# Kernel tuning notes

Hardware: AMD Instinct MI355X
Metric: run time of the kernel (lower is better)

## Reference

```python
import jax, jax.numpy as jnp
import numpy as np

NUM_EXPERTS = 64
TOP_K = 8
NUM_TOKENS = 8192
HIDDEN = 1024
INTER = 512


def setup_inputs() -> dict:
    key = jax.random.key(0)
    k1, k2, k3, k4 = jax.random.split(key, 4)
    # 0.02 scale keeps activations in a sane range (randn weights with fan-in 1024)
    return {
        "hidden_states": jax.random.normal(k1, (NUM_TOKENS, HIDDEN), jnp.float32),
        "router_weight": jax.random.normal(k2, (HIDDEN, NUM_EXPERTS), jnp.float32) * 0.02,
        "merged_gate_up_proj": jax.random.normal(k3, (NUM_EXPERTS, HIDDEN, 2 * INTER), jnp.float32) * 0.02,
        "merged_down_proj": jax.random.normal(k4, (NUM_EXPERTS, INTER, HIDDEN), jnp.float32) * 0.02,
    }


def reference(hidden_states, router_weight, merged_gate_up_proj, merged_down_proj):
    T, H = hidden_states.shape
    E = router_weight.shape[1]

    # ---- Router: softmax over experts, top-k, renormalize top-k weights ----
    logits = hidden_states @ router_weight                       # [T, E]
    probs = jax.nn.softmax(logits, axis=-1)
    routing_weights, routing_indices = jax.lax.top_k(probs, TOP_K)  # [T, k]
    routing_weights = routing_weights / routing_weights.sum(-1, keepdims=True)

    # ---- Permute (haojun_permute_topk): replicate tokens topk times, stable-sort by expert ----
    flat_indices = routing_indices.reshape(-1)                   # [T*k]
    sort_order = jnp.argsort(flat_indices)                       # stable sort
    flat_states = jnp.repeat(hidden_states, TOP_K, axis=0)       # [T*k, H]
    permuted = flat_states[sort_order]                           # tokens grouped by expert
    group_sizes = jnp.bincount(flat_indices, length=E).astype(jnp.int32)  # tokens per expert

    # ---- Grouped MLP (grouped_gemm.gmm equivalent): y_i = x_i @ W[expert(i)] ----
    merged = jax.lax.ragged_dot(permuted, merged_gate_up_proj, group_sizes)  # [T*k, 2*I]
    gate, up = jnp.split(merged, 2, axis=-1)
    h = jax.nn.silu(gate) * up                                   # SiLU-gated (hidden_act='silu')
    expert_out = jax.lax.ragged_dot(h, merged_down_proj, group_sizes)        # [T*k, H]

    # ---- Unpermute: invert the sort, weight by routing probs, sum over top-k ----
    inv = jnp.argsort(sort_order)                                # unsort_order
    unpermuted = expert_out[inv].reshape(T, TOP_K, H)
    return (unpermuted * routing_weights[..., None]).sum(axis=1)  # [T, H]
```

## Files before the change

### kernel.cpp

```cpp
#include <hip/hip_runtime.h>
#include <cstdint>
#include <cstddef>

typedef __bf16 bf16_t;
typedef __bf16 bf16x8 __attribute__((ext_vector_type(8)));
typedef __bf16 bf16x4 __attribute__((ext_vector_type(4)));
typedef float f32x4 __attribute__((ext_vector_type(4)));

#define T_TOKENS 8192
#define HID 1024
#define INTER 512
#define NEXP 64
#define TOPK 8
#define NROWS (T_TOKENS * TOPK)
#define RT_TOK 16

typedef const unsigned int __attribute__((address_space(1)))* gptr_t;
typedef unsigned int __attribute__((address_space(3)))* lptr_t;

__device__ __forceinline__ void gload_lds16(const void* g, void* l) {
  __builtin_amdgcn_global_load_lds((gptr_t)g, (lptr_t)l, 16, 0, 0);
}

__device__ __forceinline__ f32x4 mfma16(bf16x8 a, bf16x8 b, f32x4 c) {
  return __builtin_amdgcn_mfma_f32_16x16x32_bf16(a, b, c, 0, 0, 0);
}

__device__ __forceinline__ int xcd_swizzle(int bid, int nwg) {
  int q = nwg >> 3;
  int xcd = bid & 7, i = bid >> 3;
  return xcd * q + i;
}

__global__ void transpose_cvt_kernel(const float* __restrict__ W, bf16_t* __restrict__ Wt,
                                     int K, int N) {
  const int e = blockIdx.z;
  const int n0 = blockIdx.x * 64, k0 = blockIdx.y * 64;
  const int tid = threadIdx.x;
  __shared__ __align__(8) bf16_t tile[64][68];
  {
    const int r = tid >> 2, cq = tid & 3;
    const float* src = W + ((size_t)e * K + k0 + r) * N + n0 + cq * 16;
#pragma unroll
    for (int q = 0; q < 4; ++q) {
      float4 v = *(const float4*)(src + q * 4);
      bf16x4 b;
      b[0] = (bf16_t)v.x; b[1] = (bf16_t)v.y; b[2] = (bf16_t)v.z; b[3] = (bf16_t)v.w;
      *(bf16x4*)&tile[r][cq * 16 + q * 4] = b;
    }
  }
  __syncthreads();
  {
    const int nl = tid >> 2, kq = tid & 3;
    __align__(16) bf16_t tmp[16];
#pragma unroll
    for (int i = 0; i < 16; ++i) tmp[i] = tile[kq * 16 + i][nl];
    bf16_t* dst = Wt + ((size_t)e * N + n0 + nl) * K + k0 + kq * 16;
    *(bf16x8*)(dst + 0) = *(const bf16x8*)(tmp + 0);
    *(bf16x8*)(dst + 8) = *(const bf16x8*)(tmp + 8);
  }
}

__global__ void cvt_bf16_kernel(const float* __restrict__ in, bf16_t* __restrict__ out, int n4) {
  int i = blockIdx.x * blockDim.x + threadIdx.x;
  if (i < n4) {
    float4 v = ((const float4*)in)[i];
    bf16x4 o;
    o[0] = (bf16_t)v.x; o[1] = (bf16_t)v.y; o[2] = (bf16_t)v.z; o[3] = (bf16_t)v.w;
    ((bf16x4*)out)[i] = o;
  }
}

__launch_bounds__(256, 2)
__global__ void router_kernel(const float* __restrict__ hs, const float* __restrict__ rw,
                              float* __restrict__ wval, int* __restrict__ widx) {
  const int t0 = blockIdx.x * RT_TOK;
  const int tid = threadIdx.x;
  const int lane = tid & 63, w = tid >> 6;
  __shared__ float hsl[RT_TOK][HID / 4][4];
  __shared__ float part[4][RT_TOK][NEXP];

  for (int i = tid; i < RT_TOK * (HID / 4); i += 256) {
    int t = i >> 8, c = i & 255;
    *(float4*)&hsl[t][c][0] = ((const float4*)(hs + (size_t)(t0 + t) * HID))[c];
  }
  __syncthreads();

  float acc[RT_TOK];
#pragma unroll
  for (int t = 0; t < RT_TOK; ++t) acc[t] = 0.f;
  const int kb = w * 256;
  for (int kc = 0; kc < 64; ++kc) {
    const int k = kb + kc * 4;
    float r0 = rw[(size_t)(k + 0) * NEXP + lane];
    float r1 = rw[(size_t)(k + 1) * NEXP + lane];
    float r2 = rw[(size_t)(k + 2) * NEXP + lane];
    float r3 = rw[(size_t)(k + 3) * NEXP + lane];
#pragma unroll
    for (int t = 0; t < RT_TOK; ++t) {
      float4 hv = *(const float4*)&hsl[t][(kb >> 2) + kc][0];
      acc[t] = fmaf(hv.x, r0, acc[t]);
      acc[t] = fmaf(hv.y, r1, acc[t]);
      acc[t] = fmaf(hv.z, r2, acc[t]);
      acc[t] = fmaf(hv.w, r3, acc[t]);
    }
  }
#pragma unroll
  for (int t = 0; t < RT_TOK; ++t) part[w][t][lane] = acc[t];
  __syncthreads();

  for (int j = 0; j < 4; ++j) {
    const int t = w * 4 + j;
    float logit = part[0][t][lane] + part[1][t][lane] + part[2][t][lane] + part[3][t][lane];
    float m = logit;
    for (int off = 32; off; off >>= 1) m = fmaxf(m, __shfl_xor(m, off));
    float ex = expf(logit - m);
    float Z = ex;
    for (int off = 32; off; off >>= 1) Z += __shfl_xor(Z, off);
    float p = ex / Z;
    float sum8 = 0.f;
    float outv[8]; int outi[8];
#pragma unroll
    for (int s = 0; s < 8; ++s) {
      float v = p; int idx = lane;
      for (int off = 32; off; off >>= 1) {
        float vv = __shfl_xor(v, off);
        int ii = __shfl_xor(idx, off);
        if (vv > v || (vv == v && ii < idx)) { v = vv; idx = ii; }
      }
      outv[s] = v; outi[s] = idx; sum8 += v;
      if (lane == idx) p = -1.f;
    }
    if (lane == 0) {
      float inv = 1.f / sum8;
#pragma unroll
      for (int s = 0; s < 8; ++s) {
        wval[(size_t)(t0 + t) * TOPK + s] = outv[s] * inv;
        widx[(size_t)(t0 + t) * TOPK + s] = outi[s];
      }
    }
  }
}

__global__ void hist_kernel(const int* __restrict__ widx, int* __restrict__ cnt) {
  __shared__ int h[NEXP];
  if (threadIdx.x < NEXP) h[threadIdx.x] = 0;
  __syncthreads();
  for (int i = blockIdx.x * blockDim.x + threadIdx.x; i < NROWS; i += gridDim.x * blockDim.x)
    atomicAdd(&h[widx[i]], 1);
  __syncthreads();
  if (threadIdx.x < NEXP) atomicAdd(&cnt[threadIdx.x], h[threadIdx.x]);
}

__global__ void scan_kernel(const int* __restrict__ cnt, int* __restrict__ seg,
                            int* __restrict__ cnt2) {
  if (threadIdx.x == 0) {
    int a = 0;
    for (int e2 = 0; e2 < NEXP; ++e2) { seg[e2] = a; a += cnt[e2]; }
    seg[NEXP] = a;
  }
  if (threadIdx.x < NEXP) cnt2[threadIdx.x] = 0;
}

__global__ void assign_kernel(const int* __restrict__ widx, const int* __restrict__ seg,
                              int* __restrict__ cnt2, int* __restrict__ row_org) {
  for (int i = blockIdx.x * blockDim.x + threadIdx.x; i < NROWS; i += gridDim.x * blockDim.x) {
    int e = widx[i];
    int p = seg[e] + atomicAdd(&cnt2[e], 1);
    row_org[p] = i;
  }
}

__launch_bounds__(256, 2)
__global__ void gemm1_kernel(const bf16_t* __restrict__ hb, const bf16_t* __restrict__ Wt1,
                             const int* __restrict__ row_org, const int* __restrict__ seg,
                             bf16_t* __restrict__ h) {
  const int bid = blockIdx.x + gridDim.x * (blockIdx.y + gridDim.y * blockIdx.z);
  const int swz = xcd_swizzle(bid, 16 * 4 * NEXP);
  const int mt = swz & 15;
  const int nt = (swz >> 4) & 3;
  const int e = swz >> 6;

  const int ms = seg[e];
  const int sz = seg[e + 1] - ms;
  const int n0 = nt * 128;
  const int tid = threadIdx.x;
  const int lane = tid & 63;
  const int wid = tid >> 6;
  const int wm = wid >> 1, wn = wid & 1;
  __shared__ __align__(16) bf16_t As[128 * 64];
  __shared__ __align__(16) bf16_t Bs[256 * 64];

  const int srow = tid >> 3;
  const int cg = (tid & 7) ^ (srow & 7);

  size_t boff[8];
#pragma unroll
  for (int b = 0; b < 8; ++b) {
    int brow = b * 32 + srow;
    int n = (brow < 128) ? (n0 + brow) : (512 + n0 + (brow - 128));
    boff[b] = ((size_t)e * 1024 + n) * 1024 + cg * 8;
  }
  const int l15 = lane & 15, l4 = lane >> 4;

  for (int m0 = mt * 128; m0 < sz; m0 += 16 * 128) {
    size_t aoff[4];
#pragma unroll
    for (int a = 0; a < 4; ++a) {
      int row = a * 32 + srow;
      int idx = m0 + row; if (idx >= sz) idx = sz - 1;
      aoff[a] = (size_t)(row_org[ms + idx] >> 3) * HID + cg * 8;
    }
    f32x4 accg[4][4], accu[4][4];
#pragma unroll
    for (int mi = 0; mi < 4; ++mi)
#pragma unroll
      for (int ni = 0; ni < 4; ++ni) {
        accg[mi][ni] = (f32x4){0.f, 0.f, 0.f, 0.f};
        accu[mi][ni] = (f32x4){0.f, 0.f, 0.f, 0.f};
      }

    for (int kt = 0; kt < 16; ++kt) {
      const int ko = kt * 64;
      __syncthreads();
#pragma unroll
      for (int a = 0; a < 4; ++a)
        gload_lds16(hb + aoff[a] + ko, (char*)As + a * 4096 + tid * 16);
#pragma unroll
      for (int b = 0; b < 8; ++b)
        gload_lds16(Wt1 + boff[b] + ko, (char*)Bs + b * 4096 + tid * 16);
      __syncthreads();
#pragma unroll
      for (int kf = 0; kf < 2; ++kf) {
        const int ch = kf * 4 + l4;
        bf16x8 af[4], bg[4], bu[4];
#pragma unroll
        for (int mi = 0; mi < 4; ++mi) {
          int r = wm * 64 + mi * 16 + l15;
          af[mi] = *(const bf16x8*)((const char*)As + r * 128 + ((ch ^ (r & 7)) << 4));
        }
#pragma unroll
        for (int ni = 0; ni < 4; ++ni) {
          int rg = wn * 64 + ni * 16 + l15;
          bg[ni] = *(const bf16x8*)((const char*)Bs + rg * 128 + ((ch ^ (rg & 7)) << 4));
          int ru = rg + 128;
          bu[ni] = *(const bf16x8*)((const char*)Bs + ru * 128 + ((ch ^ (ru & 7)) << 4));
        }
#pragma unroll
        for (int mi = 0; mi < 4; ++mi)
#pragma unroll
          for (int ni = 0; ni < 4; ++ni) {
            accg[mi][ni] = mfma16(af[mi], bg[ni], accg[mi][ni]);
            accu[mi][ni] = mfma16(af[mi], bu[ni], accu[mi][ni]);
          }
      }
    }
#pragma unroll
    for (int mi = 0; mi < 4; ++mi) {
#pragma unroll
      for (int j = 0; j < 4; ++j) {
        int mrow = wm * 64 + mi * 16 + l4 * 4 + j;
        int idx = m0 + mrow;
        if (idx < sz) {
          bf16_t* hrow = h + (size_t)(ms + idx) * INTER + n0 + wn * 64 + l15;
#pragma unroll
          for (int ni = 0; ni < 4; ++ni) {
            float g = accg[mi][ni][j];
            float u = accu[mi][ni][j];
            float s = g / (1.f + __expf(-g));
            hrow[ni * 16] = (bf16_t)(s * u);
          }
        }
      }
    }
  }
}

__launch_bounds__(256, 2)
__global__ void gemm2_kernel(const bf16_t* __restrict__ h, const bf16_t* __restrict__ Wt2,
                             const int* __restrict__ row_org, const int* __restrict__ seg,
                             bf16_t* __restrict__ eo) {
  const int bid = blockIdx.x + gridDim.x * (blockIdx.y + gridDim.y * blockIdx.z);
  const int swz = xcd_swizzle(bid, 16 * 8 * NEXP);
  const int mt = swz & 15;
  const int nt = (swz >> 4) & 7;
  const int e = swz >> 7;

  const int ms = seg[e];
  const int sz = seg[e + 1] - ms;
  const int n0 = nt * 128;
  const int tid = threadIdx.x;
  const int lane = tid & 63;
  const int wid = tid >> 6;
  const int wm = wid >> 1, wn = wid & 1;
  __shared__ __align__(16) bf16_t As[128 * 64];
  __shared__ __align__(16) bf16_t Bs[128 * 64];
  const int srow = tid >> 3;
  const int cg = (tid & 7) ^ (srow & 7);
  size_t boff[4];
#pragma unroll
  for (int b = 0; b < 4; ++b) {
    int brow = b * 32 + srow;
    boff[b] = ((size_t)e * 1024 + n0 + brow) * INTER + cg * 8;
  }
  const int l15 = lane & 15, l4 = lane >> 4;

  for (int m0 = mt * 128; m0 < sz; m0 += 16 * 128) {
    size_t aoff[4];
#pragma unroll
    for (int a = 0; a < 4; ++a) {
      int row = a * 32 + srow;
      int idx = m0 + row; if (idx >= sz) idx = sz - 1;
      aoff[a] = (size_t)(ms + idx) * INTER + cg * 8;
    }
    f32x4 acc[4][4];
#pragma unroll
    for (int mi = 0; mi < 4; ++mi)
#pragma unroll
      for (int ni = 0; ni < 4; ++ni) acc[mi][ni] = (f32x4){0.f, 0.f, 0.f, 0.f};

    for (int kt = 0; kt < 8; ++kt) {
      const int ko = kt * 64;
      __syncthreads();
#pragma unroll
      for (int a = 0; a < 4; ++a)
        gload_lds16(h + aoff[a] + ko, (char*)As + a * 4096 + tid * 16);
#pragma unroll
      for (int b = 0; b < 4; ++b)
        gload_lds16(Wt2 + boff[b] + ko, (char*)Bs + b * 4096 + tid * 16);
      __syncthreads();
#pragma unroll
      for (int kf = 0; kf < 2; ++kf) {
        const int ch = kf * 4 + l4;
        bf16x8 af[4], bb[4];
#pragma unroll
        for (int mi = 0; mi < 4; ++mi) {
          int r = wm * 64 + mi * 16 + l15;
          af[mi] = *(const bf16x8*)((const char*)As + r * 128 + ((ch ^ (r & 7)) << 4));
        }
#pragma unroll
        for (int ni = 0; ni < 4; ++ni) {
          int r = wn * 64 + ni * 16 + l15;
          bb[ni] = *(const bf16x8*)((const char*)Bs + r * 128 + ((ch ^ (r & 7)) << 4));
        }
#pragma unroll
        for (int mi = 0; mi < 4; ++mi)
#pragma unroll
          for (int ni = 0; ni < 4; ++ni)
            acc[mi][ni] = mfma16(af[mi], bb[ni], acc[mi][ni]);
      }
    }
#pragma unroll
    for (int mi = 0; mi < 4; ++mi) {
#pragma unroll
      for (int j = 0; j < 4; ++j) {
        int mrow = wm * 64 + mi * 16 + l4 * 4 + j;
        int idx = m0 + mrow;
        if (idx < sz) {
          int org = row_org[ms + idx];
          bf16_t* orow = eo + (size_t)org * HID + n0 + wn * 64 + l15;
#pragma unroll
          for (int ni = 0; ni < 4; ++ni)
            orow[ni * 16] = (bf16_t)acc[mi][ni][j];
        }
      }
    }
  }
}

__global__ void unpermute_kernel(const bf16_t* __restrict__ eo, const float* __restrict__ wval,
                                 float* __restrict__ out) {
  const int t = blockIdx.x;
  const int c0 = threadIdx.x * 8;
  float w[8];
#pragma unroll
  for (int s = 0; s < 8; ++s) w[s] = wval[(size_t)t * 8 + s];
  float acc[8] = {0.f, 0.f, 0.f, 0.f, 0.f, 0.f, 0.f, 0.f};
#pragma unroll
  for (int s = 0; s < 8; ++s) {
    bf16x8 v = *(const bf16x8*)(eo + ((size_t)t * 8 + s) * HID + c0);
#pragma unroll
    for (int q = 0; q < 8; ++q) acc[q] = fmaf(w[s], (float)v[q], acc[q]);
  }
  *(float4*)(out + (size_t)t * HID + c0) = *(float4*)&acc[0];
  *(float4*)(out + (size_t)t * HID + c0 + 4) = *(float4*)&acc[4];
}

extern "C" void kernel_launch(void* const* d_in, const int* in_sizes, int n_in,
                              void* d_out, int out_size, void* d_ws, size_t ws_size,
                              hipStream_t stream) {
  (void)in_sizes; (void)n_in; (void)ws_size; (void)out_size;
  const float* hs = (const float*)d_in[0];
  const float* rw = (const float*)d_in[1];
  const float* w1 = (const float*)d_in[2];
  const float* w2 = (const float*)d_in[3];
  float* out = (float*)d_out;

  char* p = (char*)d_ws;
  size_t off = 0;
  auto carve = [&](size_t bytes) {
    void* r = p + off;
    off = (off + bytes + 255) & ~(size_t)255;
    return r;
  };
  bf16_t* Wt1  = (bf16_t*)carve((size_t)NEXP * 1024 * 1024 * 2);
  bf16_t* Wt2  = (bf16_t*)carve((size_t)NEXP * 1024 * 512 * 2);
  bf16_t* hb   = (bf16_t*)carve((size_t)T_TOKENS * HID * 2);
  bf16_t* hmid = (bf16_t*)carve((size_t)NROWS * INTER * 2);
  float* wval  = (float*)carve((size_t)NROWS * 4);
  int* widx    = (int*)carve((size_t)NROWS * 4);
  int* row_org = (int*)carve((size_t)NROWS * 4);
  int* cnt     = (int*)carve(256);
  int* seg     = (int*)carve(66 * 4);
  int* cnt2    = (int*)carve(256);

  bf16_t* eo = Wt1;

  (void)hipMemsetAsync(cnt, 0, 256, stream);

  transpose_cvt_kernel<<<dim3(16, 16, NEXP), 256, 0, stream>>>(w1, Wt1, 1024, 1024);
  transpose_cvt_kernel<<<dim3(16, 8, NEXP), 256, 0, stream>>>(w2, Wt2, 512, 1024);
  cvt_bf16_kernel<<<(T_TOKENS * HID / 4 + 255) / 256, 256, 0, stream>>>(hs, hb, T_TOKENS * HID / 4);
  router_kernel<<<T_TOKENS / RT_TOK, 256, 0, stream>>>(hs, rw, wval, widx);
  hist_kernel<<<128, 256, 0, stream>>>(widx, cnt);
  scan_kernel<<<1, 64, 0, stream>>>(cnt, seg, cnt2);
  assign_kernel<<<128, 256, 0, stream>>>(widx, seg, cnt2, row_org);
  gemm1_kernel<<<dim3(16, 4, NEXP), 256, 0, stream>>>(hb, Wt1, row_org, seg, hmid);
  gemm2_kernel<<<dim3(16, 8, NEXP), 256, 0, stream>>>(hmid, Wt2, row_org, seg, eo);
  unpermute_kernel<<<T_TOKENS, 128, 0, stream>>>(eo, wval, out);
}
```

Before: 612.4 us.

## Double-buffer grouped GEMM tiles, narrow N tiles, fuse cvt and histogram into router

The two grouped GEMMs now double-buffer their LDS A/B tiles, so the next K-slice's global-to-LDS loads are issued before computing the current one, with explicit vmcnt waits and barriers. N tiles shrink from 128 to 64 columns and the grid is reshaped (8 M-slots by more N tiles), which keeps LDS within budget and changes the per-expert parallelism. The bf16 conversion of hidden states and the expert histogram are folded into the router kernel, removing two launches and one extra pass over the activations. The hand-written vmcnt counts must match the number of loads issued per stage. Narrower N tiles lower MFMA reuse per A-tile load.

```diff
diff --git a/kernel.cpp b/kernel.cpp
--- a/kernel.cpp
+++ b/kernel.cpp
@@ -61,28 +61,25 @@
   }
 }
 
-__global__ void cvt_bf16_kernel(const float* __restrict__ in, bf16_t* __restrict__ out, int n4) {
-  int i = blockIdx.x * blockDim.x + threadIdx.x;
-  if (i < n4) {
-    float4 v = ((const float4*)in)[i];
-    bf16x4 o;
-    o[0] = (bf16_t)v.x; o[1] = (bf16_t)v.y; o[2] = (bf16_t)v.z; o[3] = (bf16_t)v.w;
-    ((bf16x4*)out)[i] = o;
-  }
-}
-
 __launch_bounds__(256, 2)
 __global__ void router_kernel(const float* __restrict__ hs, const float* __restrict__ rw,
-                              float* __restrict__ wval, int* __restrict__ widx) {
+                              float* __restrict__ wval, int* __restrict__ widx,
+                              bf16_t* __restrict__ hb, int* __restrict__ cnt) {
   const int t0 = blockIdx.x * RT_TOK;
   const int tid = threadIdx.x;
   const int lane = tid & 63, w = tid >> 6;
   __shared__ float hsl[RT_TOK][HID / 4][4];
   __shared__ float part[4][RT_TOK][NEXP];
+  __shared__ int bh[NEXP];
+  if (tid < NEXP) bh[tid] = 0;
 
   for (int i = tid; i < RT_TOK * (HID / 4); i += 256) {
     int t = i >> 8, c = i & 255;
-    *(float4*)&hsl[t][c][0] = ((const float4*)(hs + (size_t)(t0 + t) * HID))[c];
+    float4 v = ((const float4*)(hs + (size_t)(t0 + t) * HID))[c];
+    *(float4*)&hsl[t][c][0] = v;
+    bf16x4 o;
+    o[0] = (bf16_t)v.x; o[1] = (bf16_t)v.y; o[2] = (bf16_t)v.z; o[3] = (bf16_t)v.w;
+    *(bf16x4*)(hb + (size_t)(t0 + t) * HID + c * 4) = o;
   }
   __syncthreads();
 
@@ -137,19 +134,12 @@
       for (int s = 0; s < 8; ++s) {
         wval[(size_t)(t0 + t) * TOPK + s] = outv[s] * inv;
         widx[(size_t)(t0 + t) * TOPK + s] = outi[s];
-      }
-    }
-  }
-}
-
-__global__ void hist_kernel(const int* __restrict__ widx, int* __restrict__ cnt) {
-  __shared__ int h[NEXP];
-  if (threadIdx.x < NEXP) h[threadIdx.x] = 0;
+        atomicAdd(&bh[outi[s]], 1);
+      }
+    }
+  }
   __syncthreads();
-  for (int i = blockIdx.x * blockDim.x + threadIdx.x; i < NROWS; i += gridDim.x * blockDim.x)
-    atomicAdd(&h[widx[i]], 1);
-  __syncthreads();
-  if (threadIdx.x < NEXP) atomicAdd(&cnt[threadIdx.x], h[threadIdx.x]);
+  if (tid < NEXP) atomicAdd(&cnt[tid], bh[tid]);
 }
 
 __global__ void scan_kernel(const int* __restrict__ cnt, int* __restrict__ seg,
@@ -176,34 +166,34 @@
                              const int* __restrict__ row_org, const int* __restrict__ seg,
                              bf16_t* __restrict__ h) {
   const int bid = blockIdx.x + gridDim.x * (blockIdx.y + gridDim.y * blockIdx.z);
-  const int swz = xcd_swizzle(bid, 16 * 4 * NEXP);
-  const int mt = swz & 15;
-  const int nt = (swz >> 4) & 3;
+  const int swz = xcd_swizzle(bid, 8 * 8 * NEXP);
+  const int mt = swz & 7;
+  const int nt = (swz >> 3) & 7;
   const int e = swz >> 6;
 
   const int ms = seg[e];
   const int sz = seg[e + 1] - ms;
-  const int n0 = nt * 128;
+  const int n0 = nt * 64;
   const int tid = threadIdx.x;
   const int lane = tid & 63;
   const int wid = tid >> 6;
   const int wm = wid >> 1, wn = wid & 1;
-  __shared__ __align__(16) bf16_t As[128 * 64];
-  __shared__ __align__(16) bf16_t Bs[256 * 64];
+  __shared__ __align__(16) bf16_t As[2][128 * 64];
+  __shared__ __align__(16) bf16_t Bs[2][128 * 64];
 
   const int srow = tid >> 3;
   const int cg = (tid & 7) ^ (srow & 7);
 
-  size_t boff[8];
-#pragma unroll
-  for (int b = 0; b < 8; ++b) {
+  size_t boff[4];
+#pragma unroll
+  for (int b = 0; b < 4; ++b) {
     int brow = b * 32 + srow;
-    int n = (brow < 128) ? (n0 + brow) : (512 + n0 + (brow - 128));
+    int n = (brow < 64) ? (n0 + brow) : (512 + n0 + (brow - 64));
     boff[b] = ((size_t)e * 1024 + n) * 1024 + cg * 8;
   }
   const int l15 = lane & 15, l4 = lane >> 4;
 
-  for (int m0 = mt * 128; m0 < sz; m0 += 16 * 128) {
+  for (int m0 = mt * 128; m0 < sz; m0 += 8 * 128) {
     size_t aoff[4];
 #pragma unroll
     for (int a = 0; a < 4; ++a) {
@@ -211,49 +201,59 @@
       int idx = m0 + row; if (idx >= sz) idx = sz - 1;
       aoff[a] = (size_t)(row_org[ms + idx] >> 3) * HID + cg * 8;
     }
-    f32x4 accg[4][4], accu[4][4];
+    f32x4 accg[4][2], accu[4][2];
 #pragma unroll
     for (int mi = 0; mi < 4; ++mi)
 #pragma unroll
-      for (int ni = 0; ni < 4; ++ni) {
+      for (int ni = 0; ni < 2; ++ni) {
         accg[mi][ni] = (f32x4){0.f, 0.f, 0.f, 0.f};
         accu[mi][ni] = (f32x4){0.f, 0.f, 0.f, 0.f};
       }
 
+    auto stage = [&](int buf, int ko) {
+#pragma unroll
+      for (int a = 0; a < 4; ++a)
+        gload_lds16(hb + aoff[a] + ko, (char*)&As[buf][0] + a * 4096 + tid * 16);
+#pragma unroll
+      for (int b = 0; b < 4; ++b)
+        gload_lds16(Wt1 + boff[b] + ko, (char*)&Bs[buf][0] + b * 4096 + tid * 16);
+    };
+
+    stage(0, 0);
+    int cur = 0;
     for (int kt = 0; kt < 16; ++kt) {
-      const int ko = kt * 64;
-      __syncthreads();
-#pragma unroll
-      for (int a = 0; a < 4; ++a)
-        gload_lds16(hb + aoff[a] + ko, (char*)As + a * 4096 + tid * 16);
-#pragma unroll
-      for (int b = 0; b < 8; ++b)
-        gload_lds16(Wt1 + boff[b] + ko, (char*)Bs + b * 4096 + tid * 16);
-      __syncthreads();
+      if (kt < 15) {
+        stage(cur ^ 1, (kt + 1) * 64);
+        asm volatile("s_waitcnt vmcnt(8)\n\ts_barrier" ::: "memory");
+      } else {
+        asm volatile("s_waitcnt vmcnt(0)\n\ts_barrier" ::: "memory");
+      }
 #pragma unroll
       for (int kf = 0; kf < 2; ++kf) {
         const int ch = kf * 4 + l4;
-        bf16x8 af[4], bg[4], bu[4];
+        bf16x8 af[4], bg[2], bu[2];
 #pragma unroll
         for (int mi = 0; mi < 4; ++mi) {
           int r = wm * 64 + mi * 16 + l15;
-          af[mi] = *(const bf16x8*)((const char*)As + r * 128 + ((ch ^ (r & 7)) << 4));
-        }
-#pragma unroll
-        for (int ni = 0; ni < 4; ++ni) {
-          int rg = wn * 64 + ni * 16 + l15;
-          bg[ni] = *(const bf16x8*)((const char*)Bs + rg * 128 + ((ch ^ (rg & 7)) << 4));
-          int ru = rg + 128;
-          bu[ni] = *(const bf16x8*)((const char*)Bs + ru * 128 + ((ch ^ (ru & 7)) << 4));
+          af[mi] = *(const bf16x8*)((const char*)&As[cur][0] + r * 128 + ((ch ^ (r & 7)) << 4));
+        }
+#pragma unroll
+        for (int ni = 0; ni < 2; ++ni) {
+          int rg = wn * 32 + ni * 16 + l15;
+          bg[ni] = *(const bf16x8*)((const char*)&Bs[cur][0] + rg * 128 + ((ch ^ (rg & 7)) << 4));
+          int ru = rg + 64;
+          bu[ni] = *(const bf16x8*)((const char*)&Bs[cur][0] + ru * 128 + ((ch ^ (ru & 7)) << 4));
         }
 #pragma unroll
         for (int mi = 0; mi < 4; ++mi)
 #pragma unroll
-          for (int ni = 0; ni < 4; ++ni) {
+          for (int ni = 0; ni < 2; ++ni) {
             accg[mi][ni] = mfma16(af[mi], bg[ni], accg[mi][ni]);
             accu[mi][ni] = mfma16(af[mi], bu[ni], accu[mi][ni]);
           }
       }
+      asm volatile("s_barrier" ::: "memory");
+      cur ^= 1;
     }
 #pragma unroll
     for (int mi = 0; mi < 4; ++mi) {
@@ -262,9 +262,9 @@
         int mrow = wm * 64 + mi * 16 + l4 * 4 + j;
         int idx = m0 + mrow;
         if (idx < sz) {
-          bf16_t* hrow = h + (size_t)(ms + idx) * INTER + n0 + wn * 64 + l15;
-#pragma unroll
-          for (int ni = 0; ni < 4; ++ni) {
+          bf16_t* hrow = h + (size_t)(ms + idx) * INTER + n0 + wn * 32 + l15;
+#pragma unroll
+          for (int ni = 0; ni < 2; ++ni) {
             float g = accg[mi][ni][j];
             float u = accu[mi][ni][j];
             float s = g / (1.f + __expf(-g));
@@ -281,31 +281,31 @@
                              const int* __restrict__ row_org, const int* __restrict__ seg,
                              bf16_t* __restrict__ eo) {
   const int bid = blockIdx.x + gridDim.x * (blockIdx.y + gridDim.y * blockIdx.z);
-  const int swz = xcd_swizzle(bid, 16 * 8 * NEXP);
-  const int mt = swz & 15;
-  const int nt = (swz >> 4) & 7;
+  const int swz = xcd_swizzle(bid, 8 * 16 * NEXP);
+  const int mt = swz & 7;
+  const int nt = (swz >> 3) & 15;
   const int e = swz >> 7;
 
   const int ms = seg[e];
   const int sz = seg[e + 1] - ms;
-  const int n0 = nt * 128;
+  const int n0 = nt * 64;
   const int tid = threadIdx.x;
   const int lane = tid & 63;
   const int wid = tid >> 6;
   const int wm = wid >> 1, wn = wid & 1;
-  __shared__ __align__(16) bf16_t As[128 * 64];
-  __shared__ __align__(16) bf16_t Bs[128 * 64];
+  __shared__ __align__(16) bf16_t As[2][128 * 64];
+  __shared__ __align__(16) bf16_t Bs[2][64 * 64];
   const int srow = tid >> 3;
   const int cg = (tid & 7) ^ (srow & 7);
-  size_t boff[4];
-#pragma unroll
-  for (int b = 0; b < 4; ++b) {
+  size_t boff[2];
+#pragma unroll
+  for (int b = 0; b < 2; ++b) {
     int brow = b * 32 + srow;
     boff[b] = ((size_t)e * 1024 + n0 + brow) * INTER + cg * 8;
   }
   const int l15 = lane & 15, l4 = lane >> 4;
 
-  for (int m0 = mt * 128; m0 < sz; m0 += 16 * 128) {
+  for (int m0 = mt * 128; m0 < sz; m0 += 8 * 128) {
     size_t aoff[4];
 #pragma unroll
     for (int a = 0; a < 4; ++a) {
@@ -313,42 +313,52 @@
       int idx = m0 + row; if (idx >= sz) idx = sz - 1;
       aoff[a] = (size_t)(ms + idx) * INTER + cg * 8;
     }
-    f32x4 acc[4][4];
+    f32x4 acc[4][2];
 #pragma unroll
     for (int mi = 0; mi < 4; ++mi)
 #pragma unroll
-      for (int ni = 0; ni < 4; ++ni) acc[mi][ni] = (f32x4){0.f, 0.f, 0.f, 0.f};
-
+      for (int ni = 0; ni < 2; ++ni) acc[mi][ni] = (f32x4){0.f, 0.f, 0.f, 0.f};
+
+    auto stage = [&](int buf, int ko) {
+#pragma unroll
+      for (int a = 0; a < 4; ++a)
+        gload_lds16(h + aoff[a] + ko, (char*)&As[buf][0] + a * 4096 + tid * 16);
+#pragma unroll
+      for (int b = 0; b < 2; ++b)
+        gload_lds16(Wt2 + boff[b] + ko, (char*)&Bs[buf][0] + b * 4096 + tid * 16);
+    };
+
+    stage(0, 0);
+    int cur = 0;
     for (int kt = 0; kt < 8; ++kt) {
-      const int ko = kt * 64;
-      __syncthreads();
-#pragma unroll
-      for (int a = 0; a < 4; ++a)
-        gload_lds16(h + aoff[a] + ko, (char*)As + a * 4096 + tid * 16);
-#pragma unroll
-      for (int b = 0; b < 4; ++b)
-        gload_lds16(Wt2 + boff[b] + ko, (char*)Bs + b * 4096 + tid * 16);
-      __syncthreads();
+      if (kt < 7) {
+        stage(cur ^ 1, (kt + 1) * 64);
+        asm volatile("s_waitcnt vmcnt(6)\n\ts_barrier" ::: "memory");
+      } else {
+        asm volatile("s_waitcnt vmcnt(0)\n\ts_barrier" ::: "memory");
+      }
 #pragma unroll
       for (int kf = 0; kf < 2; ++kf) {
         const int ch = kf * 4 + l4;
-        bf16x8 af[4], bb[4];
+        bf16x8 af[4], bb[2];
 #pragma unroll
         for (int mi = 0; mi < 4; ++mi) {
           int r = wm * 64 + mi * 16 + l15;
-          af[mi] = *(const bf16x8*)((const char*)As + r * 128 + ((ch ^ (r & 7)) << 4));
-        }
-#pragma unroll
-        for (int ni = 0; ni < 4; ++ni) {
-          int r = wn * 64 + ni * 16 + l15;
-          bb[ni] = *(const bf16x8*)((const char*)Bs + r * 128 + ((ch ^ (r & 7)) << 4));
+          af[mi] = *(const bf16x8*)((const char*)&As[cur][0] + r * 128 + ((ch ^ (r & 7)) << 4));
+        }
+#pragma unroll
+        for (int ni = 0; ni < 2; ++ni) {
+          int r = wn * 32 + ni * 16 + l15;
+          bb[ni] = *(const bf16x8*)((const char*)&Bs[cur][0] + r * 128 + ((ch ^ (r & 7)) << 4));
         }
 #pragma unroll
         for (int mi = 0; mi < 4; ++mi)
 #pragma unroll
-          for (int ni = 0; ni < 4; ++ni)
+          for (int ni = 0; ni < 2; ++ni)
             acc[mi][ni] = mfma16(af[mi], bb[ni], acc[mi][ni]);
       }
+      asm volatile("s_barrier" ::: "memory");
+      cur ^= 1;
     }
 #pragma unroll
     for (int mi = 0; mi < 4; ++mi) {
@@ -358,9 +368,9 @@
         int idx = m0 + mrow;
         if (idx < sz) {
           int org = row_org[ms + idx];
-          bf16_t* orow = eo + (size_t)org * HID + n0 + wn * 64 + l15;
-#pragma unroll
-          for (int ni = 0; ni < 4; ++ni)
+          bf16_t* orow = eo + (size_t)org * HID + n0 + wn * 32 + l15;
+#pragma unroll
+          for (int ni = 0; ni < 2; ++ni)
             orow[ni * 16] = (bf16_t)acc[mi][ni][j];
         }
       }
@@ -420,12 +430,10 @@
 
   transpose_cvt_kernel<<<dim3(16, 16, NEXP), 256, 0, stream>>>(w1, Wt1, 1024, 1024);
   transpose_cvt_kernel<<<dim3(16, 8, NEXP), 256, 0, stream>>>(w2, Wt2, 512, 1024);
-  cvt_bf16_kernel<<<(T_TOKENS * HID / 4 + 255) / 256, 256, 0, stream>>>(hs, hb, T_TOKENS * HID / 4);
-  router_kernel<<<T_TOKENS / RT_TOK, 256, 0, stream>>>(hs, rw, wval, widx);
-  hist_kernel<<<128, 256, 0, stream>>>(widx, cnt);
+  router_kernel<<<T_TOKENS / RT_TOK, 256, 0, stream>>>(hs, rw, wval, widx, hb, cnt);
   scan_kernel<<<1, 64, 0, stream>>>(cnt, seg, cnt2);
   assign_kernel<<<128, 256, 0, stream>>>(widx, seg, cnt2, row_org);
-  gemm1_kernel<<<dim3(16, 4, NEXP), 256, 0, stream>>>(hb, Wt1, row_org, seg, hmid);
-  gemm2_kernel<<<dim3(16, 8, NEXP), 256, 0, stream>>>(hmid, Wt2, row_org, seg, eo);
+  gemm1_kernel<<<dim3(8, 8, NEXP), 256, 0, stream>>>(hb, Wt1, row_org, seg, hmid);
+  gemm2_kernel<<<dim3(8, 16, NEXP), 256, 0, stream>>>(hmid, Wt2, row_org, seg, eo);
   unpermute_kernel<<<T_TOKENS, 128, 0, stream>>>(eo, wval, out);
 }
```

New measurement: 778.0 us. 1.27x slower.

## Fuse preprocessing kernels: merge weight transposes, fold cast and histogram into router

Applied to the files above, without the earlier changes.

Merges the two weight transpose/convert launches into one grid that also zeroes the counters, which replaces the memset. Folds the hidden-state bf16 conversion and the per-expert histogram into the router kernel, and moves the prefix scan into each assign block. Unpermute now handles two tokens per 256-thread block. The goal is to cut launch count, one extra read of the hidden states, and small serial kernels, at the cost of redundant scans in every assign block and shared-memory atomics in the router.

```diff
diff --git a/kernel.cpp b/kernel.cpp
--- a/kernel.cpp
+++ b/kernel.cpp
@@ -32,11 +32,22 @@
   return xcd * q + i;
 }
 
-__global__ void transpose_cvt_kernel(const float* __restrict__ W, bf16_t* __restrict__ Wt,
-                                     int K, int N) {
+__global__ void transpose_cvt2_kernel(const float* __restrict__ w1, bf16_t* __restrict__ Wt1,
+                                      const float* __restrict__ w2, bf16_t* __restrict__ Wt2,
+                                      int* __restrict__ cntz) {
+  const int tid = threadIdx.x;
+  if (blockIdx.x == 0 && blockIdx.y == 0 && blockIdx.z == 0 && tid < 128) cntz[tid] = 0;
+
   const int e = blockIdx.z;
-  const int n0 = blockIdx.x * 64, k0 = blockIdx.y * 64;
-  const int tid = threadIdx.x;
+  const float* W; bf16_t* Wt; int K, k0;
+  if (blockIdx.y < 16) {
+    W = w1; Wt = Wt1; K = 1024; k0 = blockIdx.y * 64;
+  } else {
+    W = w2; Wt = Wt2; K = 512; k0 = (blockIdx.y - 16) * 64;
+  }
+  const int N = 1024;
+  const int n0 = blockIdx.x * 64;
+
   __shared__ __align__(8) bf16_t tile[64][68];
   {
     const int r = tid >> 2, cq = tid & 3;
@@ -61,28 +72,25 @@
   }
 }
 
-__global__ void cvt_bf16_kernel(const float* __restrict__ in, bf16_t* __restrict__ out, int n4) {
-  int i = blockIdx.x * blockDim.x + threadIdx.x;
-  if (i < n4) {
-    float4 v = ((const float4*)in)[i];
-    bf16x4 o;
-    o[0] = (bf16_t)v.x; o[1] = (bf16_t)v.y; o[2] = (bf16_t)v.z; o[3] = (bf16_t)v.w;
-    ((bf16x4*)out)[i] = o;
-  }
-}
-
 __launch_bounds__(256, 2)
 __global__ void router_kernel(const float* __restrict__ hs, const float* __restrict__ rw,
-                              float* __restrict__ wval, int* __restrict__ widx) {
+                              float* __restrict__ wval, int* __restrict__ widx,
+                              bf16_t* __restrict__ hb, int* __restrict__ cnt) {
   const int t0 = blockIdx.x * RT_TOK;
   const int tid = threadIdx.x;
   const int lane = tid & 63, w = tid >> 6;
   __shared__ float hsl[RT_TOK][HID / 4][4];
   __shared__ float part[4][RT_TOK][NEXP];
+  __shared__ int bh[NEXP];
+  if (tid < NEXP) bh[tid] = 0;
 
   for (int i = tid; i < RT_TOK * (HID / 4); i += 256) {
     int t = i >> 8, c = i & 255;
-    *(float4*)&hsl[t][c][0] = ((const float4*)(hs + (size_t)(t0 + t) * HID))[c];
+    float4 v = ((const float4*)(hs + (size_t)(t0 + t) * HID))[c];
+    *(float4*)&hsl[t][c][0] = v;
+    bf16x4 o;
+    o[0] = (bf16_t)v.x; o[1] = (bf16_t)v.y; o[2] = (bf16_t)v.z; o[3] = (bf16_t)v.w;
+    *(bf16x4*)(hb + (size_t)(t0 + t) * HID + c * 4) = o;
   }
   __syncthreads();
 
@@ -137,36 +145,32 @@
       for (int s = 0; s < 8; ++s) {
         wval[(size_t)(t0 + t) * TOPK + s] = outv[s] * inv;
         widx[(size_t)(t0 + t) * TOPK + s] = outi[s];
-      }
-    }
-  }
-}
-
-__global__ void hist_kernel(const int* __restrict__ widx, int* __restrict__ cnt) {
-  __shared__ int h[NEXP];
-  if (threadIdx.x < NEXP) h[threadIdx.x] = 0;
+        atomicAdd(&bh[outi[s]], 1);
+      }
+    }
+  }
   __syncthreads();
-  for (int i = blockIdx.x * blockDim.x + threadIdx.x; i < NROWS; i += gridDim.x * blockDim.x)
-    atomicAdd(&h[widx[i]], 1);
+  if (tid < NEXP) atomicAdd(&cnt[tid], bh[tid]);
+}
+
+__global__ void assign_kernel(const int* __restrict__ widx, const int* __restrict__ cnt,
+                              int* __restrict__ cnt2, int* __restrict__ row_org,
+                              int* __restrict__ seg) {
+  __shared__ int segl[NEXP];
+  const int tid = threadIdx.x;
+  if (tid < NEXP) {
+    int a = 0;
+    for (int j = 0; j < tid; ++j) a += cnt[j];
+    segl[tid] = a;
+    if (blockIdx.x == 0) {
+      seg[tid] = a;
+      if (tid == NEXP - 1) seg[NEXP] = a + cnt[NEXP - 1];
+    }
+  }
   __syncthreads();
-  if (threadIdx.x < NEXP) atomicAdd(&cnt[threadIdx.x], h[threadIdx.x]);
-}
-
-__global__ void scan_kernel(const int* __restrict__ cnt, int* __restrict__ seg,
-                            int* __restrict__ cnt2) {
-  if (threadIdx.x == 0) {
-    int a = 0;
-    for (int e2 = 0; e2 < NEXP; ++e2) { seg[e2] = a; a += cnt[e2]; }
-    seg[NEXP] = a;
-  }
-  if (threadIdx.x < NEXP) cnt2[threadIdx.x] = 0;
-}
-
-__global__ void assign_kernel(const int* __restrict__ widx, const int* __restrict__ seg,
-                              int* __restrict__ cnt2, int* __restrict__ row_org) {
-  for (int i = blockIdx.x * blockDim.x + threadIdx.x; i < NROWS; i += gridDim.x * blockDim.x) {
+  for (int i = blockIdx.x * blockDim.x + tid; i < NROWS; i += gridDim.x * blockDim.x) {
     int e = widx[i];
-    int p = seg[e] + atomicAdd(&cnt2[e], 1);
+    int p = segl[e] + atomicAdd(&cnt2[e], 1);
     row_org[p] = i;
   }
 }
@@ -370,8 +374,8 @@
 
 __global__ void unpermute_kernel(const bf16_t* __restrict__ eo, const float* __restrict__ wval,
                                  float* __restrict__ out) {
-  const int t = blockIdx.x;
-  const int c0 = threadIdx.x * 8;
+  const int t = blockIdx.x * 2 + (threadIdx.x >> 7);
+  const int c0 = (threadIdx.x & 127) * 8;
   float w[8];
 #pragma unroll
   for (int s = 0; s < 8; ++s) w[s] = wval[(size_t)t * 8 + s];
@@ -410,22 +414,16 @@
   float* wval  = (float*)carve((size_t)NROWS * 4);
   int* widx    = (int*)carve((size_t)NROWS * 4);
   int* row_org = (int*)carve((size_t)NROWS * 4);
-  int* cnt     = (int*)carve(256);
+  int* cnt     = (int*)carve(512);
   int* seg     = (int*)carve(66 * 4);
-  int* cnt2    = (int*)carve(256);
+  int* cnt2    = cnt + 64;
 
   bf16_t* eo = Wt1;
 
-  (void)hipMemsetAsync(cnt, 0, 256, stream);
-
-  transpose_cvt_kernel<<<dim3(16, 16, NEXP), 256, 0, stream>>>(w1, Wt1, 1024, 1024);
-  transpose_cvt_kernel<<<dim3(16, 8, NEXP), 256, 0, stream>>>(w2, Wt2, 512, 1024);
-  cvt_bf16_kernel<<<(T_TOKENS * HID / 4 + 255) / 256, 256, 0, stream>>>(hs, hb, T_TOKENS * HID / 4);
-  router_kernel<<<T_TOKENS / RT_TOK, 256, 0, stream>>>(hs, rw, wval, widx);
-  hist_kernel<<<128, 256, 0, stream>>>(widx, cnt);
-  scan_kernel<<<1, 64, 0, stream>>>(cnt, seg, cnt2);
-  assign_kernel<<<128, 256, 0, stream>>>(widx, seg, cnt2, row_org);
+  transpose_cvt2_kernel<<<dim3(16, 24, 64), 256, 0, stream>>>(w1, Wt1, w2, Wt2, cnt);
+  router_kernel<<<T_TOKENS / RT_TOK, 256, 0, stream>>>(hs, rw, wval, widx, hb, cnt);
+  assign_kernel<<<128, 256, 0, stream>>>(widx, cnt, cnt2, row_org, seg);
   gemm1_kernel<<<dim3(16, 4, NEXP), 256, 0, stream>>>(hb, Wt1, row_org, seg, hmid);
   gemm2_kernel<<<dim3(16, 8, NEXP), 256, 0, stream>>>(hmid, Wt2, row_org, seg, eo);
-  unpermute_kernel<<<T_TOKENS, 128, 0, stream>>>(eo, wval, out);
-}
+  unpermute_kernel<<<T_TOKENS / 2, 256, 0, stream>>>(eo, wval, out);
+}
```

Measured after the change: 641.4 us. 1.05x slower.
